# Kernel optimization log

Hardware: AMD Instinct MI355X
Metric: run time of the kernel (lower is better)

Reference implementation:

```python
import jax, jax.numpy as jnp
import numpy as np

N_NODES = 100000
IN_DIM = 128
HIDDEN = 256
N_EDGES = 1600000


def gcn_conv(x, W, b, src, dst, n_nodes):
    """PyG GCNConv: add self-loops, symmetric deg^-1/2 normalization, linear, aggregate."""
    h = x @ W  # [N, out]
    # degrees with self-loops (edge weight 1 each)
    deg = jax.ops.segment_sum(jnp.ones_like(dst, dtype=h.dtype), dst, num_segments=n_nodes)
    dinv = jax.lax.rsqrt(jnp.maximum(deg, 1e-12))
    norm = dinv[src] * dinv[dst]  # [E+N]
    msg = h[src] * norm[:, None]  # [E+N, out]
    out = jax.ops.segment_sum(msg, dst, num_segments=n_nodes)
    return out + b


def setup_inputs() -> dict:
    key = jax.random.key(0)
    k1, k2, k3, k4 = jax.random.split(key, 4)
    x = jax.random.normal(k1, (N_NODES, IN_DIM), dtype=jnp.float32)
    edge_index = jax.random.randint(k2, (2, N_EDGES), 0, N_NODES, dtype=jnp.int64)
    # Glorot-style init for weights, zero bias (as in PyG GCNConv defaults)
    W1 = jax.random.normal(k3, (IN_DIM, HIDDEN), dtype=jnp.float32) / np.sqrt(IN_DIM)
    b1 = jnp.zeros((HIDDEN,), dtype=jnp.float32)
    W2 = jax.random.normal(k4, (HIDDEN, 1), dtype=jnp.float32) / np.sqrt(HIDDEN)
    b2 = jnp.zeros((1,), dtype=jnp.float32)
    return {"x": x, "edge_index": edge_index, "W1": W1, "b1": b1, "W2": W2, "b2": b2}


def reference(x, edge_index, W1, b1, W2, b2):
    n = x.shape[0]
    loops = jnp.arange(n, dtype=edge_index.dtype)
    src = jnp.concatenate([edge_index[0], loops])
    dst = jnp.concatenate([edge_index[1], loops])
    h = gcn_conv(x, W1, b1, src, dst, n)
    h = jax.nn.relu(h)
    # dropout p=0.5 is identity in eval mode (training=False)
    out = gcn_conv(h, W2, b2, src, dst, n)
    return out
```

## Files before the change

### kernel.cpp

```cpp
#include <hip/hip_runtime.h>
#include <hip/hip_bf16.h>


typedef __attribute__((ext_vector_type(8))) short bf16x8;
typedef __attribute__((ext_vector_type(4))) float f32x4;

#define SLOTS 48
#define NPART 8

__device__ __forceinline__ unsigned short f2bf(float f) {
  unsigned int x = __builtin_bit_cast(unsigned int, f);
  unsigned int r = x + 0x7FFFu + ((x >> 16) & 1u);
  return (unsigned short)(r >> 16);
}
__device__ __forceinline__ float bf2f(unsigned short h) {
  unsigned int x = ((unsigned int)h) << 16;
  return __builtin_bit_cast(float, x);
}

__device__ __forceinline__ long long ld_idx(const void* ei, long long i, int is64) {
  if (is64) return ((const long long*)ei)[i];
  return (long long)((const int*)ei)[i];
}

__global__ void k_detect(const void* __restrict__ ei, int E, int N, int* __restrict__ flag) {
  __shared__ int bad;
  if (threadIdx.x == 0) bad = 0;
  __syncthreads();
  int cnt = min(E, 1024);
  int lb = 0;
  for (int i = threadIdx.x; i < cnt; i += blockDim.x) {
    long long v = ((const long long*)ei)[i];
    if (v < 0 || v >= (long long)N) lb = 1;
  }
  if (lb) atomicOr(&bad, 1);
  __syncthreads();
  if (threadIdx.x == 0) *flag = bad ? 0 : 1;
}

__global__ void k_zero_i32(int* __restrict__ p, int n) {
  int i = blockIdx.x * blockDim.x + threadIdx.x;
  if (i < n) p[i] = 0;
}

__global__ void k_xq(const float4* __restrict__ X4, int4* __restrict__ Xq, int total8) {
  int i = blockIdx.x * blockDim.x + threadIdx.x;
  if (i >= total8) return;
  float4 u = X4[i * 2], v = X4[i * 2 + 1];
  int q0 = max(-32767, min(32767, __float2int_rn(u.x * 4096.f)));
  int q1 = max(-32767, min(32767, __float2int_rn(u.y * 4096.f)));
  int q2 = max(-32767, min(32767, __float2int_rn(u.z * 4096.f)));
  int q3 = max(-32767, min(32767, __float2int_rn(u.w * 4096.f)));
  int q4 = max(-32767, min(32767, __float2int_rn(v.x * 4096.f)));
  int q5 = max(-32767, min(32767, __float2int_rn(v.y * 4096.f)));
  int q6 = max(-32767, min(32767, __float2int_rn(v.z * 4096.f)));
  int q7 = max(-32767, min(32767, __float2int_rn(v.w * 4096.f)));
  int4 o;
  o.x = (q0 & 0xFFFF) | (q1 << 16);
  o.y = (q2 & 0xFFFF) | (q3 << 16);
  o.z = (q4 & 0xFFFF) | (q5 << 16);
  o.w = (q6 & 0xFFFF) | (q7 << 16);
  Xq[i] = o;
}

__global__ void k_deg(const void* __restrict__ ei, int E, int N,
                      const int* __restrict__ flag, int* __restrict__ deg,
                      int* __restrict__ bucket) {
  int p = blockIdx.x & (NPART - 1);
  int r = blockIdx.x >> 3;
  int R = gridDim.x >> 3;
  int np = (N + NPART - 1) / NPART;
  int lo = p * np, hi = min(N, lo + np);
  int is64 = *flag;
  int stride = R * blockDim.x;
  for (int e = r * blockDim.x + threadIdx.x; e < E; e += stride) {
    int d = (int)ld_idx(ei, (long long)E + e, is64);
    if (d < lo || d >= hi) continue;
    int s = (int)ld_idx(ei, e, is64);
    int slot = atomicAdd(&deg[d], 1);
    if (slot < SLOTS) bucket[(size_t)d * SLOTS + slot] = s;
  }
}

__device__ __forceinline__ void acc_i16x8(const int4 v, const float w, float* a) {
  a[0] += w * (float)(short)(v.x);
  a[1] += w * (float)(v.x >> 16);
  a[2] += w * (float)(short)(v.y);
  a[3] += w * (float)(v.y >> 16);
  a[4] += w * (float)(short)(v.z);
  a[5] += w * (float)(v.z >> 16);
  a[6] += w * (float)(short)(v.w);
  a[7] += w * (float)(v.w >> 16);
}

__global__ __launch_bounds__(256) void k_gather(
    const short* __restrict__ Xq, const int* __restrict__ bucket,
    const int* __restrict__ deg, unsigned short* __restrict__ Ahi,
    unsigned short* __restrict__ Alo, int N) {
  int g = blockIdx.x * 16 + (threadIdx.x >> 4);
  int gl = threadIdx.x & 15;
  if (g >= N) return;
  int l8 = gl * 8;
  int dg = deg[g];
  float di = rsqrtf((float)(dg + 1));
  const int* bsrc = bucket + (size_t)g * SLOTS;
  int n = min(dg, SLOTS);
  float a[8] = {0.f, 0.f, 0.f, 0.f, 0.f, 0.f, 0.f, 0.f};
  int e = 0;
  for (; e + 8 <= n; e += 8) {
    int s[8];
    int4 xv[8];
    float w[8];
    #pragma unroll
    for (int u = 0; u < 8; ++u) s[u] = bsrc[e + u];
    #pragma unroll
    for (int u = 0; u < 8; ++u)
      xv[u] = *(const int4*)(Xq + (size_t)s[u] * 128 + l8);
    #pragma unroll
    for (int u = 0; u < 8; ++u) w[u] = rsqrtf((float)(deg[s[u]] + 1));
    #pragma unroll
    for (int u = 0; u < 8; ++u) acc_i16x8(xv[u], w[u], a);
  }
  for (; e < n; ++e) {
    int s = bsrc[e];
    int4 xv = *(const int4*)(Xq + (size_t)s * 128 + l8);
    acc_i16x8(xv, rsqrtf((float)(deg[s] + 1)), a);
  }
  int4 xs = *(const int4*)(Xq + (size_t)g * 128 + l8);
  acc_i16x8(xs, di, a);
  const float S = 1.0f / 4096.0f;
  #pragma unroll
  for (int j = 0; j < 8; ++j) a[j] = di * S * a[j];
  unsigned short h[8], l[8];
  #pragma unroll
  for (int j = 0; j < 8; ++j) h[j] = f2bf(a[j]);
  #pragma unroll
  for (int j = 0; j < 8; ++j) l[j] = f2bf(a[j] - bf2f(h[j]));
  int4 hv, lv;
  hv.x = (unsigned)h[0] | ((unsigned)h[1] << 16);
  hv.y = (unsigned)h[2] | ((unsigned)h[3] << 16);
  hv.z = (unsigned)h[4] | ((unsigned)h[5] << 16);
  hv.w = (unsigned)h[6] | ((unsigned)h[7] << 16);
  lv.x = (unsigned)l[0] | ((unsigned)l[1] << 16);
  lv.y = (unsigned)l[2] | ((unsigned)l[3] << 16);
  lv.z = (unsigned)l[4] | ((unsigned)l[5] << 16);
  lv.w = (unsigned)l[6] | ((unsigned)l[7] << 16);
  *(int4*)(Ahi + (size_t)g * 128 + l8) = hv;
  *(int4*)(Alo + (size_t)g * 128 + l8) = lv;
}

__global__ void k_w1prep(const float* __restrict__ W1, int4* __restrict__ Bpk) {
  int tid = blockIdx.x * 256 + threadIdx.x;
  int lane = tid & 63, ks = (tid >> 6) & 3, ct = tid >> 8;
  int c = ct >> 2, fi = (ct & 3) * 4 + ks;
  int kbase = ks * 32 + (lane >> 4) * 8;
  int col = ct * 16 + (lane & 15);
  unsigned short h[8], lo[8];
  #pragma unroll
  for (int j = 0; j < 8; ++j) {
    float w = W1[(size_t)(kbase + j) * 256 + col];
    h[j] = f2bf(w);
    lo[j] = f2bf(w - bf2f(h[j]));
  }
  int4 hv, lv;
  hv.x = (unsigned)h[0] | ((unsigned)h[1] << 16);
  hv.y = (unsigned)h[2] | ((unsigned)h[3] << 16);
  hv.z = (unsigned)h[4] | ((unsigned)h[5] << 16);
  hv.w = (unsigned)h[6] | ((unsigned)h[7] << 16);
  lv.x = (unsigned)lo[0] | ((unsigned)lo[1] << 16);
  lv.y = (unsigned)lo[2] | ((unsigned)lo[3] << 16);
  lv.z = (unsigned)lo[4] | ((unsigned)lo[5] << 16);
  lv.w = (unsigned)lo[6] | ((unsigned)lo[7] << 16);
  Bpk[c * 2048 + fi * 64 + lane] = hv;
  Bpk[c * 2048 + 1024 + fi * 64 + lane] = lv;
}

__global__ __launch_bounds__(256) void k_gemm_mfma(
    const unsigned short* __restrict__ Ahi, const unsigned short* __restrict__ Alo,
    const int4* __restrict__ Bpk, const float* __restrict__ b1,
    const float* __restrict__ W2, const int* __restrict__ deg,
    float* __restrict__ zs, int N) {
  __shared__ int4 lb[2][2048];
  int tid = threadIdx.x;
  int wv = tid >> 6, lane = tid & 63;
  int m0 = (blockIdx.x * 4 + wv) * 32;
  if (m0 > N - 32) m0 = N - 32;
  int cl = lane & 15, g = lane >> 4;

  for (int i = tid; i < 2048; i += 256) lb[0][i] = Bpk[i];

  const bf16x8* arh0 = (const bf16x8*)(Ahi + (size_t)(m0 + cl) * 128 + g * 8);
  const bf16x8* arl0 = (const bf16x8*)(Alo + (size_t)(m0 + cl) * 128 + g * 8);
  const bf16x8* arh1 = (const bf16x8*)(Ahi + (size_t)(m0 + 16 + cl) * 128 + g * 8);
  const bf16x8* arl1 = (const bf16x8*)(Alo + (size_t)(m0 + 16 + cl) * 128 + g * 8);
  bf16x8 ah0[4], al0[4], ah1[4], al1[4];
  #pragma unroll
  for (int ks = 0; ks < 4; ++ks) {
    ah0[ks] = arh0[ks * 4];
    al0[ks] = arl0[ks * 4];
    ah1[ks] = arh1[ks * 4];
    al1[ks] = arl1[ks * 4];
  }

  f32x4 acc0[16], acc1[16];
  #pragma unroll
  for (int ct = 0; ct < 16; ++ct) {
    acc0[ct] = (f32x4){0.f, 0.f, 0.f, 0.f};
    acc1[ct] = (f32x4){0.f, 0.f, 0.f, 0.f};
  }

  #pragma unroll
  for (int c = 0; c < 4; ++c) {
    __syncthreads();
    if (c < 3) {
      for (int i = tid; i < 2048; i += 256) lb[(c + 1) & 1][i] = Bpk[(c + 1) * 2048 + i];
    }
    const int4* lbuf = lb[c & 1];
    #pragma unroll
    for (int ks = 0; ks < 4; ++ks) {
      #pragma unroll
      for (int i = 0; i < 4; ++i) {
        int ct = c * 4 + i;
        int fi = i * 4 + ks;
        bf16x8 bh = __builtin_bit_cast(bf16x8, lbuf[fi * 64 + lane]);
        bf16x8 bl = __builtin_bit_cast(bf16x8, lbuf[1024 + fi * 64 + lane]);
        acc0[ct] = __builtin_amdgcn_mfma_f32_16x16x32_bf16(ah0[ks], bh, acc0[ct], 0, 0, 0);
        acc0[ct] = __builtin_amdgcn_mfma_f32_16x16x32_bf16(ah0[ks], bl, acc0[ct], 0, 0, 0);
        acc0[ct] = __builtin_amdgcn_mfma_f32_16x16x32_bf16(al0[ks], bh, acc0[ct], 0, 0, 0);
        acc1[ct] = __builtin_amdgcn_mfma_f32_16x16x32_bf16(ah1[ks], bh, acc1[ct], 0, 0, 0);
        acc1[ct] = __builtin_amdgcn_mfma_f32_16x16x32_bf16(ah1[ks], bl, acc1[ct], 0, 0, 0);
        acc1[ct] = __builtin_amdgcn_mfma_f32_16x16x32_bf16(al1[ks], bh, acc1[ct], 0, 0, 0);
      }
    }
  }

  float p0 = 0.f, p1 = 0.f, p2 = 0.f, p3 = 0.f;
  float q0 = 0.f, q1 = 0.f, q2 = 0.f, q3 = 0.f;
  #pragma unroll
  for (int ct = 0; ct < 16; ++ct) {
    float bb = b1[ct * 16 + cl];
    float ww = W2[ct * 16 + cl];
    p0 += fmaxf(acc0[ct][0] + bb, 0.f) * ww;
    p1 += fmaxf(acc0[ct][1] + bb, 0.f) * ww;
    p2 += fmaxf(acc0[ct][2] + bb, 0.f) * ww;
    p3 += fmaxf(acc0[ct][3] + bb, 0.f) * ww;
    q0 += fmaxf(acc1[ct][0] + bb, 0.f) * ww;
    q1 += fmaxf(acc1[ct][1] + bb, 0.f) * ww;
    q2 += fmaxf(acc1[ct][2] + bb, 0.f) * ww;
    q3 += fmaxf(acc1[ct][3] + bb, 0.f) * ww;
  }
  #pragma unroll
  for (int s = 1; s < 16; s <<= 1) {
    p0 += __shfl_xor(p0, s); p1 += __shfl_xor(p1, s);
    p2 += __shfl_xor(p2, s); p3 += __shfl_xor(p3, s);
    q0 += __shfl_xor(q0, s); q1 += __shfl_xor(q1, s);
    q2 += __shfl_xor(q2, s); q3 += __shfl_xor(q3, s);
  }
  float pv = (cl == 0) ? p0 : (cl == 1) ? p1 : (cl == 2) ? p2 : p3;
  float qv = (cl == 0) ? q0 : (cl == 1) ? q1 : (cl == 2) ? q2 : q3;
  if (cl < 4) {
    int n0 = m0 + 4 * g + cl, n1 = n0 + 16;
    zs[n0] = rsqrtf((float)(deg[n0] + 1)) * pv;
    zs[n1] = rsqrtf((float)(deg[n1] + 1)) * qv;
  }
}

__global__ void k_outgather(const int* __restrict__ bucket, const int* __restrict__ deg,
                            const float* __restrict__ zs, const float* __restrict__ b2,
                            float* __restrict__ out, int N) {
  int i = blockIdx.x * blockDim.x + threadIdx.x;
  if (i >= N) return;
  int dg = deg[i];
  float di = rsqrtf((float)(dg + 1));
  float acc = zs[i];
  const int* bsrc = bucket + (size_t)i * SLOTS;
  int n = min(dg, SLOTS);
  int e = 0;
  float a0 = 0.f, a1 = 0.f, a2 = 0.f, a3 = 0.f;
  for (; e + 4 <= n; e += 4) {
    int s0 = bsrc[e], s1 = bsrc[e + 1], s2 = bsrc[e + 2], s3 = bsrc[e + 3];
    a0 += zs[s0]; a1 += zs[s1]; a2 += zs[s2]; a3 += zs[s3];
  }
  for (; e < n; ++e) a0 += zs[bsrc[e]];
  acc += (a0 + a1) + (a2 + a3);
  out[i] = di * acc + b2[0];
}

extern "C" void kernel_launch(void* const* d_in, const int* in_sizes, int n_in,
                              void* d_out, int out_size, void* d_ws, size_t ws_size,
                              hipStream_t stream) {
  const float* x  = (const float*)d_in[0];
  const void*  ei = d_in[1];
  const float* W1 = (const float*)d_in[2];
  const float* b1 = (const float*)d_in[3];
  const float* W2 = (const float*)d_in[4];
  const float* b2 = (const float*)d_in[5];
  float* out = (float*)d_out;

  int N = in_sizes[0] / 128;
  int E = in_sizes[1] / 2;

  char* ws = (char*)d_ws;
  size_t o = 0;
  unsigned short* Ahi = (unsigned short*)(ws + o); o += (size_t)N * 128 * 2;
  unsigned short* Alo = (unsigned short*)(ws + o); o += (size_t)N * 128 * 2;
  short* Xq = (short*)(ws + o); o += (size_t)N * 128 * 2;
  int* bucket = (int*)(ws + o); o += (size_t)N * SLOTS * 4;
  o = (o + 255) & ~(size_t)255;
  int* deg = (int*)(ws + o); o += (size_t)N * 4;
  int* flag = (int*)(ws + o); o += 4;
  o = (o + 255) & ~(size_t)255;
  float* zs = (float*)(ws + o); o += (size_t)N * 4;
  o = (o + 255) & ~(size_t)255;
  int4* Bpk = (int4*)(ws + o); o += 131072;

  k_detect<<<1, 256, 0, stream>>>(ei, E, N, flag);
  k_zero_i32<<<(N + 255) / 256, 256, 0, stream>>>(deg, N);
  k_xq<<<(N * 16 + 255) / 256, 256, 0, stream>>>((const float4*)x, (int4*)Xq, N * 16);
  k_w1prep<<<16, 256, 0, stream>>>(W1, Bpk);
  k_deg<<<2048, 256, 0, stream>>>(ei, E, N, flag, deg, bucket);
  k_gather<<<(N + 15) / 16, 256, 0, stream>>>(Xq, bucket, deg, Ahi, Alo, N);
  k_gemm_mfma<<<(N + 127) / 128, 256, 0, stream>>>(Ahi, Alo, Bpk, b1, W2, deg, zs, N);
  k_outgather<<<(N + 255) / 256, 256, 0, stream>>>(bucket, deg, zs, b2, out, N);
}
```

Baseline: 297.4 us.

## Fuse neighbor gather into MFMA GEMM and merge prep kernels into one launch

The gather kernel and the MFMA GEMM become one kernel. Each wave aggregates 16 rows in registers, splits them into bf16 hi/lo, and feeds them straight to the MFMAs, so the Ahi/Alo intermediate buffers are never written or read back. The detect, zero, quantize and W1-pack kernels are merged into one block-indexed prep launch to cut launch overhead. Index loads use nontemporal hints. In exchange, each lane now gathers a full 128-element row slice per neighbour in a strided pattern, which raises register use and may cut occupancy or hurt gather coalescing. The LDS for B is single-buffered with extra syncs.

```diff
diff --git a/kernel.cpp b/kernel.cpp
--- a/kernel.cpp
+++ b/kernel.cpp
@@ -4,6 +4,7 @@
 
 typedef __attribute__((ext_vector_type(8))) short bf16x8;
 typedef __attribute__((ext_vector_type(4))) float f32x4;
+typedef __attribute__((ext_vector_type(4))) int i32x4;
 
 #define SLOTS 48
 #define NPART 8
@@ -17,50 +18,80 @@
   unsigned int x = ((unsigned int)h) << 16;
   return __builtin_bit_cast(float, x);
 }
-
 __device__ __forceinline__ long long ld_idx(const void* ei, long long i, int is64) {
   if (is64) return ((const long long*)ei)[i];
   return (long long)((const int*)ei)[i];
 }
-
-__global__ void k_detect(const void* __restrict__ ei, int E, int N, int* __restrict__ flag) {
-  __shared__ int bad;
-  if (threadIdx.x == 0) bad = 0;
-  __syncthreads();
-  int cnt = min(E, 1024);
-  int lb = 0;
-  for (int i = threadIdx.x; i < cnt; i += blockDim.x) {
-    long long v = ((const long long*)ei)[i];
-    if (v < 0 || v >= (long long)N) lb = 1;
-  }
-  if (lb) atomicOr(&bad, 1);
-  __syncthreads();
-  if (threadIdx.x == 0) *flag = bad ? 0 : 1;
-}
-
-__global__ void k_zero_i32(int* __restrict__ p, int n) {
-  int i = blockIdx.x * blockDim.x + threadIdx.x;
-  if (i < n) p[i] = 0;
-}
-
-__global__ void k_xq(const float4* __restrict__ X4, int4* __restrict__ Xq, int total8) {
-  int i = blockIdx.x * blockDim.x + threadIdx.x;
-  if (i >= total8) return;
-  float4 u = X4[i * 2], v = X4[i * 2 + 1];
-  int q0 = max(-32767, min(32767, __float2int_rn(u.x * 4096.f)));
-  int q1 = max(-32767, min(32767, __float2int_rn(u.y * 4096.f)));
-  int q2 = max(-32767, min(32767, __float2int_rn(u.z * 4096.f)));
-  int q3 = max(-32767, min(32767, __float2int_rn(u.w * 4096.f)));
-  int q4 = max(-32767, min(32767, __float2int_rn(v.x * 4096.f)));
-  int q5 = max(-32767, min(32767, __float2int_rn(v.y * 4096.f)));
-  int q6 = max(-32767, min(32767, __float2int_rn(v.z * 4096.f)));
-  int q7 = max(-32767, min(32767, __float2int_rn(v.w * 4096.f)));
-  int4 o;
-  o.x = (q0 & 0xFFFF) | (q1 << 16);
-  o.y = (q2 & 0xFFFF) | (q3 << 16);
-  o.z = (q4 & 0xFFFF) | (q5 << 16);
-  o.w = (q6 & 0xFFFF) | (q7 << 16);
-  Xq[i] = o;
+__device__ __forceinline__ long long ld_idx_nt(const void* ei, long long i, int is64) {
+  if (is64) return __builtin_nontemporal_load(((const long long*)ei) + i);
+  return (long long)__builtin_nontemporal_load(((const int*)ei) + i);
+}
+
+__global__ __launch_bounds__(256) void k_prep(
+    const float4* __restrict__ X4, const float* __restrict__ W1,
+    const void* __restrict__ ei, int E, int N, int4* __restrict__ Xq,
+    int4* __restrict__ Bpk, int* __restrict__ deg, int* __restrict__ flag, int Gx) {
+  int b = blockIdx.x;
+  if (b < Gx) {
+    int i = b * 256 + threadIdx.x;
+    if (i < N * 16) {
+      float4 u = X4[i * 2], v = X4[i * 2 + 1];
+      int q0 = max(-32767, min(32767, __float2int_rn(u.x * 4096.f)));
+      int q1 = max(-32767, min(32767, __float2int_rn(u.y * 4096.f)));
+      int q2 = max(-32767, min(32767, __float2int_rn(u.z * 4096.f)));
+      int q3 = max(-32767, min(32767, __float2int_rn(u.w * 4096.f)));
+      int q4 = max(-32767, min(32767, __float2int_rn(v.x * 4096.f)));
+      int q5 = max(-32767, min(32767, __float2int_rn(v.y * 4096.f)));
+      int q6 = max(-32767, min(32767, __float2int_rn(v.z * 4096.f)));
+      int q7 = max(-32767, min(32767, __float2int_rn(v.w * 4096.f)));
+      int4 o;
+      o.x = (q0 & 0xFFFF) | (q1 << 16);
+      o.y = (q2 & 0xFFFF) | (q3 << 16);
+      o.z = (q4 & 0xFFFF) | (q5 << 16);
+      o.w = (q6 & 0xFFFF) | (q7 << 16);
+      Xq[i] = o;
+    }
+  } else if (b < Gx + 16) {
+    int tid = (b - Gx) * 256 + threadIdx.x;
+    int lane = tid & 63, ks = (tid >> 6) & 3, ct = tid >> 8;
+    int c = ct >> 2, fi = (ct & 3) * 4 + ks;
+    int kbase = ks * 32 + (lane >> 4) * 8;
+    int col = ct * 16 + (lane & 15);
+    unsigned short h[8], lo[8];
+    #pragma unroll
+    for (int j = 0; j < 8; ++j) {
+      float w = W1[(size_t)(kbase + j) * 256 + col];
+      h[j] = f2bf(w);
+      lo[j] = f2bf(w - bf2f(h[j]));
+    }
+    int4 hv, lv;
+    hv.x = (unsigned)h[0] | ((unsigned)h[1] << 16);
+    hv.y = (unsigned)h[2] | ((unsigned)h[3] << 16);
+    hv.z = (unsigned)h[4] | ((unsigned)h[5] << 16);
+    hv.w = (unsigned)h[6] | ((unsigned)h[7] << 16);
+    lv.x = (unsigned)lo[0] | ((unsigned)lo[1] << 16);
+    lv.y = (unsigned)lo[2] | ((unsigned)lo[3] << 16);
+    lv.z = (unsigned)lo[4] | ((unsigned)lo[5] << 16);
+    lv.w = (unsigned)lo[6] | ((unsigned)lo[7] << 16);
+    Bpk[c * 2048 + fi * 64 + lane] = hv;
+    Bpk[c * 2048 + 1024 + fi * 64 + lane] = lv;
+  } else if (b == Gx + 16) {
+    __shared__ int bad;
+    if (threadIdx.x == 0) bad = 0;
+    __syncthreads();
+    int cnt = min(E, 1024);
+    int lb = 0;
+    for (int i = threadIdx.x; i < cnt; i += blockDim.x) {
+      long long v = ((const long long*)ei)[i];
+      if (v < 0 || v >= (long long)N) lb = 1;
+    }
+    if (lb) atomicOr(&bad, 1);
+    __syncthreads();
+    if (threadIdx.x == 0) *flag = bad ? 0 : 1;
+  } else {
+    int i = (b - Gx - 17) * 256 + threadIdx.x;
+    if (i < N) deg[i] = 0;
+  }
 }
 
 __global__ void k_deg(const void* __restrict__ ei, int E, int N,
@@ -74,194 +105,165 @@
   int is64 = *flag;
   int stride = R * blockDim.x;
   for (int e = r * blockDim.x + threadIdx.x; e < E; e += stride) {
-    int d = (int)ld_idx(ei, (long long)E + e, is64);
+    int d = (int)ld_idx_nt(ei, (long long)E + e, is64);
     if (d < lo || d >= hi) continue;
-    int s = (int)ld_idx(ei, e, is64);
+    int s = (int)ld_idx_nt(ei, e, is64);
     int slot = atomicAdd(&deg[d], 1);
     if (slot < SLOTS) bucket[(size_t)d * SLOTS + slot] = s;
   }
 }
 
-__device__ __forceinline__ void acc_i16x8(const int4 v, const float w, float* a) {
-  a[0] += w * (float)(short)(v.x);
-  a[1] += w * (float)(v.x >> 16);
-  a[2] += w * (float)(short)(v.y);
-  a[3] += w * (float)(v.y >> 16);
-  a[4] += w * (float)(short)(v.z);
-  a[5] += w * (float)(v.z >> 16);
-  a[6] += w * (float)(short)(v.w);
-  a[7] += w * (float)(v.w >> 16);
-}
-
-__global__ __launch_bounds__(256) void k_gather(
+struct RowQ { i32x4 v0, v1, v2, v3; };
+__device__ __forceinline__ RowQ load_row(const short* __restrict__ Xq, int s, int g8) {
+  const short* p = Xq + (size_t)s * 128 + g8;
+  RowQ r;
+  r.v0 = *(const i32x4*)(p);
+  r.v1 = *(const i32x4*)(p + 32);
+  r.v2 = *(const i32x4*)(p + 64);
+  r.v3 = *(const i32x4*)(p + 96);
+  return r;
+}
+__device__ __forceinline__ void acc8(const i32x4 v, const float w, float* a) {
+  a[0] += w * (float)(short)(v[0]);
+  a[1] += w * (float)(v[0] >> 16);
+  a[2] += w * (float)(short)(v[1]);
+  a[3] += w * (float)(v[1] >> 16);
+  a[4] += w * (float)(short)(v[2]);
+  a[5] += w * (float)(v[2] >> 16);
+  a[6] += w * (float)(short)(v[3]);
+  a[7] += w * (float)(v[3] >> 16);
+}
+__device__ __forceinline__ void acc_row(const RowQ& r, float w, float* a) {
+  acc8(r.v0, w, a);
+  acc8(r.v1, w, a + 8);
+  acc8(r.v2, w, a + 16);
+  acc8(r.v3, w, a + 24);
+}
+
+__global__ __launch_bounds__(256) void k_gg(
     const short* __restrict__ Xq, const int* __restrict__ bucket,
-    const int* __restrict__ deg, unsigned short* __restrict__ Ahi,
-    unsigned short* __restrict__ Alo, int N) {
-  int g = blockIdx.x * 16 + (threadIdx.x >> 4);
-  int gl = threadIdx.x & 15;
-  if (g >= N) return;
-  int l8 = gl * 8;
-  int dg = deg[g];
+    const int* __restrict__ deg, const int4* __restrict__ Bpk,
+    const float* __restrict__ b1, const float* __restrict__ W2,
+    float* __restrict__ zs, int N) {
+  __shared__ int4 lb[2048];
+  int tid = threadIdx.x;
+  for (int i = tid; i < 2048; i += 256) lb[i] = Bpk[i];
+
+  int wv = tid >> 6, lane = tid & 63;
+  int cl = lane & 15, g = lane >> 4;
+  int g8 = g * 8;
+  int m0 = blockIdx.x * 64 + wv * 16;
+  if (m0 > N - 16) m0 = N - 16;
+  int row = m0 + cl;
+
+  int dg = deg[row];
   float di = rsqrtf((float)(dg + 1));
-  const int* bsrc = bucket + (size_t)g * SLOTS;
+  const int* bsrc = bucket + (size_t)row * SLOTS;
   int n = min(dg, SLOTS);
-  float a[8] = {0.f, 0.f, 0.f, 0.f, 0.f, 0.f, 0.f, 0.f};
+  float a[32];
+  #pragma unroll
+  for (int j = 0; j < 32; ++j) a[j] = 0.f;
+
   int e = 0;
-  for (; e + 8 <= n; e += 8) {
-    int s[8];
-    int4 xv[8];
-    float w[8];
+  for (; e + 4 <= n; e += 4) {
+    int s0 = __builtin_nontemporal_load(bsrc + e + 0);
+    int s1 = __builtin_nontemporal_load(bsrc + e + 1);
+    int s2 = __builtin_nontemporal_load(bsrc + e + 2);
+    int s3 = __builtin_nontemporal_load(bsrc + e + 3);
+    RowQ r0 = load_row(Xq, s0, g8);
+    RowQ r1 = load_row(Xq, s1, g8);
+    RowQ r2 = load_row(Xq, s2, g8);
+    RowQ r3 = load_row(Xq, s3, g8);
+    float w0 = rsqrtf((float)(deg[s0] + 1));
+    float w1 = rsqrtf((float)(deg[s1] + 1));
+    float w2 = rsqrtf((float)(deg[s2] + 1));
+    float w3 = rsqrtf((float)(deg[s3] + 1));
+    acc_row(r0, w0, a);
+    acc_row(r1, w1, a);
+    acc_row(r2, w2, a);
+    acc_row(r3, w3, a);
+  }
+  for (; e < n; ++e) {
+    int s = __builtin_nontemporal_load(bsrc + e);
+    RowQ r = load_row(Xq, s, g8);
+    acc_row(r, rsqrtf((float)(deg[s] + 1)), a);
+  }
+  {
+    RowQ r = load_row(Xq, row, g8);
+    acc_row(r, di, a);
+  }
+  const float S = 1.0f / 4096.0f;
+  #pragma unroll
+  for (int j = 0; j < 32; ++j) a[j] *= di * S;
+
+  bf16x8 ah[4], al[4];
+  #pragma unroll
+  for (int ks = 0; ks < 4; ++ks) {
+    unsigned short h[8], l[8];
     #pragma unroll
-    for (int u = 0; u < 8; ++u) s[u] = bsrc[e + u];
+    for (int j = 0; j < 8; ++j) h[j] = f2bf(a[ks * 8 + j]);
     #pragma unroll
-    for (int u = 0; u < 8; ++u)
-      xv[u] = *(const int4*)(Xq + (size_t)s[u] * 128 + l8);
-    #pragma unroll
-    for (int u = 0; u < 8; ++u) w[u] = rsqrtf((float)(deg[s[u]] + 1));
-    #pragma unroll
-    for (int u = 0; u < 8; ++u) acc_i16x8(xv[u], w[u], a);
-  }
-  for (; e < n; ++e) {
-    int s = bsrc[e];
-    int4 xv = *(const int4*)(Xq + (size_t)s * 128 + l8);
-    acc_i16x8(xv, rsqrtf((float)(deg[s] + 1)), a);
-  }
-  int4 xs = *(const int4*)(Xq + (size_t)g * 128 + l8);
-  acc_i16x8(xs, di, a);
-  const float S = 1.0f / 4096.0f;
-  #pragma unroll
-  for (int j = 0; j < 8; ++j) a[j] = di * S * a[j];
-  unsigned short h[8], l[8];
-  #pragma unroll
-  for (int j = 0; j < 8; ++j) h[j] = f2bf(a[j]);
-  #pragma unroll
-  for (int j = 0; j < 8; ++j) l[j] = f2bf(a[j] - bf2f(h[j]));
-  int4 hv, lv;
-  hv.x = (unsigned)h[0] | ((unsigned)h[1] << 16);
-  hv.y = (unsigned)h[2] | ((unsigned)h[3] << 16);
-  hv.z = (unsigned)h[4] | ((unsigned)h[5] << 16);
-  hv.w = (unsigned)h[6] | ((unsigned)h[7] << 16);
-  lv.x = (unsigned)l[0] | ((unsigned)l[1] << 16);
-  lv.y = (unsigned)l[2] | ((unsigned)l[3] << 16);
-  lv.z = (unsigned)l[4] | ((unsigned)l[5] << 16);
-  lv.w = (unsigned)l[6] | ((unsigned)l[7] << 16);
-  *(int4*)(Ahi + (size_t)g * 128 + l8) = hv;
-  *(int4*)(Alo + (size_t)g * 128 + l8) = lv;
-}
-
-__global__ void k_w1prep(const float* __restrict__ W1, int4* __restrict__ Bpk) {
-  int tid = blockIdx.x * 256 + threadIdx.x;
-  int lane = tid & 63, ks = (tid >> 6) & 3, ct = tid >> 8;
-  int c = ct >> 2, fi = (ct & 3) * 4 + ks;
-  int kbase = ks * 32 + (lane >> 4) * 8;
-  int col = ct * 16 + (lane & 15);
-  unsigned short h[8], lo[8];
-  #pragma unroll
-  for (int j = 0; j < 8; ++j) {
-    float w = W1[(size_t)(kbase + j) * 256 + col];
-    h[j] = f2bf(w);
-    lo[j] = f2bf(w - bf2f(h[j]));
-  }
-  int4 hv, lv;
-  hv.x = (unsigned)h[0] | ((unsigned)h[1] << 16);
-  hv.y = (unsigned)h[2] | ((unsigned)h[3] << 16);
-  hv.z = (unsigned)h[4] | ((unsigned)h[5] << 16);
-  hv.w = (unsigned)h[6] | ((unsigned)h[7] << 16);
-  lv.x = (unsigned)lo[0] | ((unsigned)lo[1] << 16);
-  lv.y = (unsigned)lo[2] | ((unsigned)lo[3] << 16);
-  lv.z = (unsigned)lo[4] | ((unsigned)lo[5] << 16);
-  lv.w = (unsigned)lo[6] | ((unsigned)lo[7] << 16);
-  Bpk[c * 2048 + fi * 64 + lane] = hv;
-  Bpk[c * 2048 + 1024 + fi * 64 + lane] = lv;
-}
-
-__global__ __launch_bounds__(256) void k_gemm_mfma(
-    const unsigned short* __restrict__ Ahi, const unsigned short* __restrict__ Alo,
-    const int4* __restrict__ Bpk, const float* __restrict__ b1,
-    const float* __restrict__ W2, const int* __restrict__ deg,
-    float* __restrict__ zs, int N) {
-  __shared__ int4 lb[2][2048];
-  int tid = threadIdx.x;
-  int wv = tid >> 6, lane = tid & 63;
-  int m0 = (blockIdx.x * 4 + wv) * 32;
-  if (m0 > N - 32) m0 = N - 32;
-  int cl = lane & 15, g = lane >> 4;
-
-  for (int i = tid; i < 2048; i += 256) lb[0][i] = Bpk[i];
-
-  const bf16x8* arh0 = (const bf16x8*)(Ahi + (size_t)(m0 + cl) * 128 + g * 8);
-  const bf16x8* arl0 = (const bf16x8*)(Alo + (size_t)(m0 + cl) * 128 + g * 8);
-  const bf16x8* arh1 = (const bf16x8*)(Ahi + (size_t)(m0 + 16 + cl) * 128 + g * 8);
-  const bf16x8* arl1 = (const bf16x8*)(Alo + (size_t)(m0 + 16 + cl) * 128 + g * 8);
-  bf16x8 ah0[4], al0[4], ah1[4], al1[4];
-  #pragma unroll
-  for (int ks = 0; ks < 4; ++ks) {
-    ah0[ks] = arh0[ks * 4];
-    al0[ks] = arl0[ks * 4];
-    ah1[ks] = arh1[ks * 4];
-    al1[ks] = arl1[ks * 4];
-  }
-
-  f32x4 acc0[16], acc1[16];
-  #pragma unroll
-  for (int ct = 0; ct < 16; ++ct) {
-    acc0[ct] = (f32x4){0.f, 0.f, 0.f, 0.f};
-    acc1[ct] = (f32x4){0.f, 0.f, 0.f, 0.f};
-  }
+    for (int j = 0; j < 8; ++j) l[j] = f2bf(a[ks * 8 + j] - bf2f(h[j]));
+    int4 hv, lv;
+    hv.x = (unsigned)h[0] | ((unsigned)h[1] << 16);
+    hv.y = (unsigned)h[2] | ((unsigned)h[3] << 16);
+    hv.z = (unsigned)h[4] | ((unsigned)h[5] << 16);
+    hv.w = (unsigned)h[6] | ((unsigned)h[7] << 16);
+    lv.x = (unsigned)l[0] | ((unsigned)l[1] << 16);
+    lv.y = (unsigned)l[2] | ((unsigned)l[3] << 16);
+    lv.z = (unsigned)l[4] | ((unsigned)l[5] << 16);
+    lv.w = (unsigned)l[6] | ((unsigned)l[7] << 16);
+    ah[ks] = __builtin_bit_cast(bf16x8, hv);
+    al[ks] = __builtin_bit_cast(bf16x8, lv);
+  }
+
+  __syncthreads();
+
+  f32x4 acc[16];
+  #pragma unroll
+  for (int ct = 0; ct < 16; ++ct) acc[ct] = (f32x4){0.f, 0.f, 0.f, 0.f};
 
   #pragma unroll
   for (int c = 0; c < 4; ++c) {
-    __syncthreads();
-    if (c < 3) {
-      for (int i = tid; i < 2048; i += 256) lb[(c + 1) & 1][i] = Bpk[(c + 1) * 2048 + i];
-    }
-    const int4* lbuf = lb[c & 1];
     #pragma unroll
     for (int ks = 0; ks < 4; ++ks) {
       #pragma unroll
       for (int i = 0; i < 4; ++i) {
         int ct = c * 4 + i;
         int fi = i * 4 + ks;
-        bf16x8 bh = __builtin_bit_cast(bf16x8, lbuf[fi * 64 + lane]);
-        bf16x8 bl = __builtin_bit_cast(bf16x8, lbuf[1024 + fi * 64 + lane]);
-        acc0[ct] = __builtin_amdgcn_mfma_f32_16x16x32_bf16(ah0[ks], bh, acc0[ct], 0, 0, 0);
-        acc0[ct] = __builtin_amdgcn_mfma_f32_16x16x32_bf16(ah0[ks], bl, acc0[ct], 0, 0, 0);
-        acc0[ct] = __builtin_amdgcn_mfma_f32_16x16x32_bf16(al0[ks], bh, acc0[ct], 0, 0, 0);
-        acc1[ct] = __builtin_amdgcn_mfma_f32_16x16x32_bf16(ah1[ks], bh, acc1[ct], 0, 0, 0);
-        acc1[ct] = __builtin_amdgcn_mfma_f32_16x16x32_bf16(ah1[ks], bl, acc1[ct], 0, 0, 0);
-        acc1[ct] = __builtin_amdgcn_mfma_f32_16x16x32_bf16(al1[ks], bh, acc1[ct], 0, 0, 0);
+        bf16x8 bh = __builtin_bit_cast(bf16x8, lb[fi * 64 + lane]);
+        bf16x8 bl = __builtin_bit_cast(bf16x8, lb[1024 + fi * 64 + lane]);
+        acc[ct] = __builtin_amdgcn_mfma_f32_16x16x32_bf16(ah[ks], bh, acc[ct], 0, 0, 0);
+        acc[ct] = __builtin_amdgcn_mfma_f32_16x16x32_bf16(ah[ks], bl, acc[ct], 0, 0, 0);
+        acc[ct] = __builtin_amdgcn_mfma_f32_16x16x32_bf16(al[ks], bh, acc[ct], 0, 0, 0);
       }
     }
+    __syncthreads();
+    if (c < 3) {
+      for (int i = tid; i < 2048; i += 256) lb[i] = Bpk[(c + 1) * 2048 + i];
+      __syncthreads();
+    }
   }
 
   float p0 = 0.f, p1 = 0.f, p2 = 0.f, p3 = 0.f;
-  float q0 = 0.f, q1 = 0.f, q2 = 0.f, q3 = 0.f;
   #pragma unroll
   for (int ct = 0; ct < 16; ++ct) {
     float bb = b1[ct * 16 + cl];
     float ww = W2[ct * 16 + cl];
-    p0 += fmaxf(acc0[ct][0] + bb, 0.f) * ww;
-    p1 += fmaxf(acc0[ct][1] + bb, 0.f) * ww;
-    p2 += fmaxf(acc0[ct][2] + bb, 0.f) * ww;
-    p3 += fmaxf(acc0[ct][3] + bb, 0.f) * ww;
-    q0 += fmaxf(acc1[ct][0] + bb, 0.f) * ww;
-    q1 += fmaxf(acc1[ct][1] + bb, 0.f) * ww;
-    q2 += fmaxf(acc1[ct][2] + bb, 0.f) * ww;
-    q3 += fmaxf(acc1[ct][3] + bb, 0.f) * ww;
+    p0 += fmaxf(acc[ct][0] + bb, 0.f) * ww;
+    p1 += fmaxf(acc[ct][1] + bb, 0.f) * ww;
+    p2 += fmaxf(acc[ct][2] + bb, 0.f) * ww;
+    p3 += fmaxf(acc[ct][3] + bb, 0.f) * ww;
   }
   #pragma unroll
   for (int s = 1; s < 16; s <<= 1) {
     p0 += __shfl_xor(p0, s); p1 += __shfl_xor(p1, s);
     p2 += __shfl_xor(p2, s); p3 += __shfl_xor(p3, s);
-    q0 += __shfl_xor(q0, s); q1 += __shfl_xor(q1, s);
-    q2 += __shfl_xor(q2, s); q3 += __shfl_xor(q3, s);
   }
   float pv = (cl == 0) ? p0 : (cl == 1) ? p1 : (cl == 2) ? p2 : p3;
-  float qv = (cl == 0) ? q0 : (cl == 1) ? q1 : (cl == 2) ? q2 : q3;
   if (cl < 4) {
-    int n0 = m0 + 4 * g + cl, n1 = n0 + 16;
+    int n0 = m0 + 4 * g + cl;
     zs[n0] = rsqrtf((float)(deg[n0] + 1)) * pv;
-    zs[n1] = rsqrtf((float)(deg[n1] + 1)) * qv;
   }
 }
 
@@ -278,10 +280,13 @@
   int e = 0;
   float a0 = 0.f, a1 = 0.f, a2 = 0.f, a3 = 0.f;
   for (; e + 4 <= n; e += 4) {
-    int s0 = bsrc[e], s1 = bsrc[e + 1], s2 = bsrc[e + 2], s3 = bsrc[e + 3];
+    int s0 = __builtin_nontemporal_load(bsrc + e + 0);
+    int s1 = __builtin_nontemporal_load(bsrc + e + 1);
+    int s2 = __builtin_nontemporal_load(bsrc + e + 2);
+    int s3 = __builtin_nontemporal_load(bsrc + e + 3);
     a0 += zs[s0]; a1 += zs[s1]; a2 += zs[s2]; a3 += zs[s3];
   }
-  for (; e < n; ++e) a0 += zs[bsrc[e]];
+  for (; e < n; ++e) a0 += zs[__builtin_nontemporal_load(bsrc + e)];
   acc += (a0 + a1) + (a2 + a3);
   out[i] = di * acc + b2[0];
 }
@@ -302,8 +307,6 @@
 
   char* ws = (char*)d_ws;
   size_t o = 0;
-  unsigned short* Ahi = (unsigned short*)(ws + o); o += (size_t)N * 128 * 2;
-  unsigned short* Alo = (unsigned short*)(ws + o); o += (size_t)N * 128 * 2;
   short* Xq = (short*)(ws + o); o += (size_t)N * 128 * 2;
   int* bucket = (int*)(ws + o); o += (size_t)N * SLOTS * 4;
   o = (o + 255) & ~(size_t)255;
@@ -314,12 +317,12 @@
   o = (o + 255) & ~(size_t)255;
   int4* Bpk = (int4*)(ws + o); o += 131072;
 
-  k_detect<<<1, 256, 0, stream>>>(ei, E, N, flag);
-  k_zero_i32<<<(N + 255) / 256, 256, 0, stream>>>(deg, N);
-  k_xq<<<(N * 16 + 255) / 256, 256, 0, stream>>>((const float4*)x, (int4*)Xq, N * 16);
-  k_w1prep<<<16, 256, 0, stream>>>(W1, Bpk);
+  int Gx = (N * 16 + 255) / 256;
+  int Gz = (N + 255) / 256;
+  int Gprep = Gx + 16 + 1 + Gz;
+  k_prep<<<Gprep, 256, 0, stream>>>((const float4*)x, W1, ei, E, N, (int4*)Xq,
+                                    Bpk, deg, flag, Gx);
   k_deg<<<2048, 256, 0, stream>>>(ei, E, N, flag, deg, bucket);
-  k_gather<<<(N + 15) / 16, 256, 0, stream>>>(Xq, bucket, deg, Ahi, Alo, N);
-  k_gemm_mfma<<<(N + 127) / 128, 256, 0, stream>>>(Ahi, Alo, Bpk, b1, W2, deg, zs, N);
+  k_gg<<<(N + 63) / 64, 256, 0, stream>>>(Xq, bucket, deg, Bpk, b1, W2, zs, N);
   k_outgather<<<(N + 255) / 256, 256, 0, stream>>>(bucket, deg, zs, b2, out, N);
 }
```

After: 307.7 us. 1.03x slower.
